# Optimization experiments

Hardware: AMD Instinct MI355X
Metric: run time of the kernel (lower is better)

The kernel has to match this reference:

```python
import jax, jax.numpy as jnp
import numpy as np

B, N, D, H = 4, 512, 64, 8
DK = D // H  # 8


def setup_inputs() -> dict:
    key = jax.random.key(0)
    ks = jax.random.split(key, 9)
    std = 0.02
    return {
        "n": jax.random.normal(ks[0], (B, N, D), dtype=jnp.float32),
        "e": jax.random.normal(ks[1], (B, N, N, D), dtype=jnp.float32),
        "W_q": jax.random.normal(ks[2], (D, D), dtype=jnp.float32) * std,
        "W_k": jax.random.normal(ks[3], (D, D), dtype=jnp.float32) * std,
        "W_v": jax.random.normal(ks[4], (D, D), dtype=jnp.float32) * std,
        "O_n": jax.random.normal(ks[5], (D, D), dtype=jnp.float32) * std,
        "W_e": jax.random.normal(ks[6], (D, H), dtype=jnp.float32) * std,
        "W_g": jax.random.normal(ks[7], (D, H), dtype=jnp.float32) * std,
        "O_e": jax.random.normal(ks[8], (H, D), dtype=jnp.float32) * std,
    }


def reference(n, e, W_q, W_k, W_v, O_n, W_e, W_g, O_e):
    b, nn_, d = n.shape
    # projections -> [B, H, N, DK]
    Q = (n @ W_q).reshape(b, nn_, H, DK).transpose(0, 2, 1, 3)
    K = (n @ W_k).reshape(b, nn_, H, DK).transpose(0, 2, 1, 3)
    V = (n @ W_v).reshape(b, nn_, H, DK).transpose(0, 2, 1, 3)
    # edge bias and gate -> [B, H, N, N]
    E = jnp.einsum('bnmd,dh->bhnm', e, W_e)
    G = jax.nn.sigmoid(jnp.einsum('bnmd,dh->bhnm', e, W_g))
    dyn_centrality = jnp.log1p(G.sum(-1))  # [B, H, N]
    # clamped scaled scores + edge bias
    A = jnp.einsum('bhnd,bhmd->bhnm', Q, K) * (DK ** -0.5)
    A = jnp.clip(A, -5.0, 5.0)
    Eb = A + E
    P = jax.nn.softmax(Eb, axis=-1)
    Vh = jnp.einsum('bhnm,bhmd->bhnd', P, V)
    Vh = Vh * dyn_centrality[..., None]
    n_out = Vh.transpose(0, 2, 1, 3).reshape(b, nn_, d) @ O_n
    e_out = jnp.einsum('bhnm,hd->bnmd', Eb, O_e)
    return n_out, e_out
```

## Files before the change

### kernel.cpp

```cpp
#include <hip/hip_runtime.h>
#include <hip/hip_bf16.h>
#include <math.h>

#define BB 4
#define NN 512
#define NP 516
#define DD 64
#define HH 8
#define DKK 8

typedef float f32x4 __attribute__((ext_vector_type(4)));
typedef short s16x8 __attribute__((ext_vector_type(8)));

__device__ __forceinline__ void split8(const float* fv, s16x8& hi, s16x8& lo) {
#pragma unroll
    for (int j = 0; j < 8; ++j) {
        const unsigned u = __float_as_uint(fv[j]);
        hi[j] = (short)(u >> 16);
        const float r = fv[j] - __uint_as_float(u & 0xFFFF0000u);
        lo[j] = (short)(__float_as_uint(r) >> 16);
    }
}

__device__ __forceinline__ short bf16rne(float f) {
    return (short)((__float_as_uint(f) + 0x8000u) >> 16);
}

__device__ __forceinline__ int swz(int r, int cb) {
    return r * 256 + (cb ^ ((r & 7) << 4));
}

__global__ __launch_bounds__(64) void qkv_kernel(
    const float* __restrict__ n,
    const float* __restrict__ Wq,
    const float* __restrict__ Wk,
    const float* __restrict__ Wv,
    float* __restrict__ Q,
    float* __restrict__ K,
    float* __restrict__ V)
{
    const int row = blockIdx.x;
    const int j = threadIdx.x;
    __shared__ __align__(16) float nr[DD];
    nr[j] = n[(size_t)row * DD + j];
    __syncthreads();
    float q = 0.f, k = 0.f, v = 0.f;
#pragma unroll
    for (int d = 0; d < DD; ++d) {
        const float nv = nr[d];
        q = fmaf(nv, Wq[d * DD + j], q);
        k = fmaf(nv, Wk[d * DD + j], k);
        v = fmaf(nv, Wv[d * DD + j], v);
    }
    Q[(size_t)row * DD + j] = q;
    K[(size_t)row * DD + j] = k;
    V[(size_t)row * DD + j] = v;
}

__global__ __launch_bounds__(64) void edge_kernel(
    const float* __restrict__ e,
    const float* __restrict__ Q,
    const float* __restrict__ K,
    const float* __restrict__ We,
    const float* __restrict__ Wg,
    const float* __restrict__ Oe,
    float* __restrict__ Ebws,
    float* __restrict__ gpartws,
    float* __restrict__ e_out)
{
    const int blk = blockIdx.x;
    const int row = blk >> 2;
    const int qtr = blk & 3;
    const int b = row >> 9;
    const int lane = threadIdx.x;
    const int cc = lane & 15;
    const int kg = lane >> 4;
    const int wr = lane >> 4;
    const int wc = (lane & 15) << 4;

    __shared__ __align__(16) char lds_e[4096];
    __shared__ __align__(16) char lds_k[4096];
    __shared__ __align__(16) char lds_o[4096];

    const float scale = 0.35355339059327373f;

    s16x8 qxh0 = {0,0,0,0,0,0,0,0}, qxh1 = {0,0,0,0,0,0,0,0};
    {
        const float* Qr = Q + (size_t)row * DD;
        if (cc == kg) {
#pragma unroll
            for (int j = 0; j < 8; ++j) qxh0[j] = bf16rne(Qr[kg * 8 + j]);
        }
        if (cc == 4 + kg) {
#pragma unroll
            for (int j = 0; j < 8; ++j) qxh1[j] = bf16rne(Qr[32 + kg * 8 + j]);
        }
    }

    s16x8 b1h0, b1l0, b1h1, b1l1;
    {
        float fv[8];
#pragma unroll
        for (int j = 0; j < 8; ++j) {
            const int k = kg * 8 + j;
            fv[j] = (cc < 8) ? We[k * HH + cc] : Wg[k * HH + (cc - 8)];
        }
        split8(fv, b1h0, b1l0);
#pragma unroll
        for (int j = 0; j < 8; ++j) {
            const int k = 32 + kg * 8 + j;
            fv[j] = (cc < 8) ? We[k * HH + cc] : Wg[k * HH + (cc - 8)];
        }
        split8(fv, b1h1, b1l1);
    }
    s16x8 b2h[4], b2l[4];
#pragma unroll
    for (int nt = 0; nt < 4; ++nt) {
        float fv[8];
#pragma unroll
        for (int j = 0; j < 8; ++j)
            fv[j] = (kg == 0) ? Oe[j * DD + nt * 16 + cc] : 0.f;
        split8(fv, b2h[nt], b2l[nt]);
    }

    float gs0 = 0.f, gs1 = 0.f, gs2 = 0.f, gs3 = 0.f;
    const float* __restrict__ e_row = e + (size_t)row * NN * DD;
    const float* __restrict__ Kb = K + (size_t)b * NN * DD;
    float* __restrict__ eo = e_out + (size_t)row * NN * DD;
    const int T0 = qtr * 8;
    const int lastT = T0 + 7;

    float4 eA0, eA1, eA2, eA3, kA0, kA1, kA2, kA3;
    float4 eB0, eB1, eB2, eB3, kB0, kB1, kB2, kB3;
    {
        const float* se = e_row + (size_t)T0 * 16 * DD + lane * 4;
        eA0 = *(const float4*)(se);        eA1 = *(const float4*)(se + 256);
        eA2 = *(const float4*)(se + 512);  eA3 = *(const float4*)(se + 768);
        const float* sk = Kb + (size_t)T0 * 16 * DD + lane * 4;
        kA0 = *(const float4*)(sk);        kA1 = *(const float4*)(sk + 256);
        kA2 = *(const float4*)(sk + 512);  kA3 = *(const float4*)(sk + 768);
        const float* se2 = e_row + (size_t)(T0 + 1) * 16 * DD + lane * 4;
        eB0 = *(const float4*)(se2);       eB1 = *(const float4*)(se2 + 256);
        eB2 = *(const float4*)(se2 + 512); eB3 = *(const float4*)(se2 + 768);
        const float* sk2 = Kb + (size_t)(T0 + 1) * 16 * DD + lane * 4;
        kB0 = *(const float4*)(sk2);       kB1 = *(const float4*)(sk2 + 256);
        kB2 = *(const float4*)(sk2 + 512); kB3 = *(const float4*)(sk2 + 768);
    }

    auto body = [&](int T,
                    float4& p0, float4& p1, float4& p2, float4& p3,
                    float4& q0, float4& q1, float4& q2, float4& q3) {
        const int m0 = T * 16;

        *(float4*)(lds_e + swz(0 + wr, wc)) = p0;
        *(float4*)(lds_e + swz(4 + wr, wc)) = p1;
        *(float4*)(lds_e + swz(8 + wr, wc)) = p2;
        *(float4*)(lds_e + swz(12 + wr, wc)) = p3;
        *(float4*)(lds_k + swz(0 + wr, wc)) = q0;
        *(float4*)(lds_k + swz(4 + wr, wc)) = q1;
        *(float4*)(lds_k + swz(8 + wr, wc)) = q2;
        *(float4*)(lds_k + swz(12 + wr, wc)) = q3;

        {
            int Tn = T + 2; if (Tn > lastT) Tn = lastT;
            const float* se = e_row + (size_t)Tn * 16 * DD + lane * 4;
            p0 = *(const float4*)(se);        p1 = *(const float4*)(se + 256);
            p2 = *(const float4*)(se + 512);  p3 = *(const float4*)(se + 768);
            const float* sk = Kb + (size_t)Tn * 16 * DD + lane * 4;
            q0 = *(const float4*)(sk);        q1 = *(const float4*)(sk + 256);
            q2 = *(const float4*)(sk + 512);  q3 = *(const float4*)(sk + 768);
        }

        const float4 ef0 = *(const float4*)(lds_e + swz(cc, kg * 32));
        const float4 ef1 = *(const float4*)(lds_e + swz(cc, kg * 32 + 16));
        const float4 ef2 = *(const float4*)(lds_e + swz(cc, 128 + kg * 32));
        const float4 ef3 = *(const float4*)(lds_e + swz(cc, 128 + kg * 32 + 16));
        const float4 kf0 = *(const float4*)(lds_k + swz(cc, kg * 32));
        const float4 kf1 = *(const float4*)(lds_k + swz(cc, kg * 32 + 16));
        const float4 kf2 = *(const float4*)(lds_k + swz(cc, 128 + kg * 32));
        const float4 kf3 = *(const float4*)(lds_k + swz(cc, 128 + kg * 32 + 16));

        s16x8 a1h0, a1h1, kh0, kh1;
        a1h0[0] = bf16rne(ef0.x); a1h0[1] = bf16rne(ef0.y);
        a1h0[2] = bf16rne(ef0.z); a1h0[3] = bf16rne(ef0.w);
        a1h0[4] = bf16rne(ef1.x); a1h0[5] = bf16rne(ef1.y);
        a1h0[6] = bf16rne(ef1.z); a1h0[7] = bf16rne(ef1.w);
        a1h1[0] = bf16rne(ef2.x); a1h1[1] = bf16rne(ef2.y);
        a1h1[2] = bf16rne(ef2.z); a1h1[3] = bf16rne(ef2.w);
        a1h1[4] = bf16rne(ef3.x); a1h1[5] = bf16rne(ef3.y);
        a1h1[6] = bf16rne(ef3.z); a1h1[7] = bf16rne(ef3.w);
        kh0[0] = bf16rne(kf0.x); kh0[1] = bf16rne(kf0.y);
        kh0[2] = bf16rne(kf0.z); kh0[3] = bf16rne(kf0.w);
        kh0[4] = bf16rne(kf1.x); kh0[5] = bf16rne(kf1.y);
        kh0[6] = bf16rne(kf1.z); kh0[7] = bf16rne(kf1.w);
        kh1[0] = bf16rne(kf2.x); kh1[1] = bf16rne(kf2.y);
        kh1[2] = bf16rne(kf2.z); kh1[3] = bf16rne(kf2.w);
        kh1[4] = bf16rne(kf3.x); kh1[5] = bf16rne(kf3.y);
        kh1[6] = bf16rne(kf3.z); kh1[7] = bf16rne(kf3.w);

        f32x4 accA = {0.f, 0.f, 0.f, 0.f};
        accA = __builtin_amdgcn_mfma_f32_16x16x32_bf16(qxh0, kh0, accA, 0, 0, 0);
        accA = __builtin_amdgcn_mfma_f32_16x16x32_bf16(qxh1, kh1, accA, 0, 0, 0);

        f32x4 accEG = {0.f, 0.f, 0.f, 0.f};
        accEG = __builtin_amdgcn_mfma_f32_16x16x32_bf16(b1h0, a1h0, accEG, 0, 0, 0);
        accEG = __builtin_amdgcn_mfma_f32_16x16x32_bf16(b1l0, a1h0, accEG, 0, 0, 0);
        accEG = __builtin_amdgcn_mfma_f32_16x16x32_bf16(b1h1, a1h1, accEG, 0, 0, 0);
        accEG = __builtin_amdgcn_mfma_f32_16x16x32_bf16(b1l1, a1h1, accEG, 0, 0, 0);

        float ebr0 = 0.f, ebr1 = 0.f, ebr2 = 0.f, ebr3 = 0.f;
        if (kg < 2) {
            const float a0 = fminf(fmaxf(accA[0] * scale, -5.f), 5.f);
            const float a1 = fminf(fmaxf(accA[1] * scale, -5.f), 5.f);
            const float a2 = fminf(fmaxf(accA[2] * scale, -5.f), 5.f);
            const float a3 = fminf(fmaxf(accA[3] * scale, -5.f), 5.f);
            ebr0 = a0 + accEG[0];
            ebr1 = a1 + accEG[1];
            ebr2 = a2 + accEG[2];
            ebr3 = a3 + accEG[3];
            const size_t base = ((size_t)row * HH + kg * 4) * NN + m0 + cc;
            Ebws[base]          = ebr0;
            Ebws[base + NN]     = ebr1;
            Ebws[base + 2 * NN] = ebr2;
            Ebws[base + 3 * NN] = ebr3;
        } else {
            gs0 += 1.f / (1.f + __expf(-accEG[0]));
            gs1 += 1.f / (1.f + __expf(-accEG[1]));
            gs2 += 1.f / (1.f + __expf(-accEG[2]));
            gs3 += 1.f / (1.f + __expf(-accEG[3]));
        }

        const float pm0 = __shfl_xor(ebr0, 16, 64);
        const float pm1 = __shfl_xor(ebr1, 16, 64);
        const float pm2 = __shfl_xor(ebr2, 16, 64);
        const float pm3 = __shfl_xor(ebr3, 16, 64);

        s16x8 a2h, a2l;
        {
            float mj[8] = {ebr0, ebr1, ebr2, ebr3, pm0, pm1, pm2, pm3};
            split8(mj, a2h, a2l);
        }
        if (lane >= 16) {
            a2h = s16x8{0, 0, 0, 0, 0, 0, 0, 0};
            a2l = s16x8{0, 0, 0, 0, 0, 0, 0, 0};
        }

#pragma unroll
        for (int nt = 0; nt < 4; ++nt) {
            f32x4 c2 = {0.f, 0.f, 0.f, 0.f};
            c2 = __builtin_amdgcn_mfma_f32_16x16x32_bf16(b2h[nt], a2h, c2, 0, 0, 0);
            c2 = __builtin_amdgcn_mfma_f32_16x16x32_bf16(b2h[nt], a2l, c2, 0, 0, 0);
            c2 = __builtin_amdgcn_mfma_f32_16x16x32_bf16(b2l[nt], a2h, c2, 0, 0, 0);
            float4 st;
            st.x = c2[0]; st.y = c2[1]; st.z = c2[2]; st.w = c2[3];
            *(float4*)(lds_o + swz(cc, nt * 64 + kg * 16)) = st;
        }

        {
            float* eob = eo + (size_t)m0 * DD + lane * 4;
            const float4 o0 = *(const float4*)(lds_o + swz(0 + wr, wc));
            const float4 o1 = *(const float4*)(lds_o + swz(4 + wr, wc));
            const float4 o2 = *(const float4*)(lds_o + swz(8 + wr, wc));
            const float4 o3 = *(const float4*)(lds_o + swz(12 + wr, wc));
            *(float4*)(eob)       = o0;
            *(float4*)(eob + 256) = o1;
            *(float4*)(eob + 512) = o2;
            *(float4*)(eob + 768) = o3;
        }
    };

#pragma unroll 1
    for (int s4 = 0; s4 < 4; ++s4) {
        body(T0 + 2 * s4,     eA0, eA1, eA2, eA3, kA0, kA1, kA2, kA3);
        body(T0 + 2 * s4 + 1, eB0, eB1, eB2, eB3, kB0, kB1, kB2, kB3);
    }

    gs0 += __shfl_xor(gs0, 1, 64); gs0 += __shfl_xor(gs0, 2, 64);
    gs0 += __shfl_xor(gs0, 4, 64); gs0 += __shfl_xor(gs0, 8, 64);
    gs1 += __shfl_xor(gs1, 1, 64); gs1 += __shfl_xor(gs1, 2, 64);
    gs1 += __shfl_xor(gs1, 4, 64); gs1 += __shfl_xor(gs1, 8, 64);
    gs2 += __shfl_xor(gs2, 1, 64); gs2 += __shfl_xor(gs2, 2, 64);
    gs2 += __shfl_xor(gs2, 4, 64); gs2 += __shfl_xor(gs2, 8, 64);
    gs3 += __shfl_xor(gs3, 1, 64); gs3 += __shfl_xor(gs3, 2, 64);
    gs3 += __shfl_xor(gs3, 4, 64); gs3 += __shfl_xor(gs3, 8, 64);
    float* gp = gpartws + ((size_t)row * 4 + qtr) * HH;
    if (lane == 32) { gp[0] = gs0; gp[1] = gs1; gp[2] = gs2; gp[3] = gs3; }
    if (lane == 48) { gp[4] = gs0; gp[5] = gs1; gp[6] = gs2; gp[7] = gs3; }
}

__global__ __launch_bounds__(256) void softmax_kernel(
    const float* __restrict__ Ebws,
    const float* __restrict__ gpartws,
    const float* __restrict__ V,
    const float* __restrict__ On,
    float* __restrict__ n_out)
{
    const int row = blockIdx.x;
    const int b = row >> 9;
    const int t = threadIdx.x;
    const int lane = t & 63;
    const int wv = t >> 6;

    __shared__ float gsum[HH];
    __shared__ float vh_lds[DD];

    if (t < HH) {
        const float* gp = gpartws + (size_t)row * 4 * HH;
        gsum[t] = gp[t] + gp[HH + t] + gp[2 * HH + t] + gp[3 * HH + t];
    }
    __syncthreads();

    const float* __restrict__ Vb = V + (size_t)b * NN * DD;
#pragma unroll
    for (int hh = 0; hh < 2; ++hh) {
        const int h = wv + hh * 4;
        const float* __restrict__ ebr = Ebws + ((size_t)row * HH + h) * NN;
        float x[8];
#pragma unroll
        for (int k = 0; k < 8; ++k) x[k] = ebr[lane + (k << 6)];
        float mx = x[0];
#pragma unroll
        for (int k = 1; k < 8; ++k) mx = fmaxf(mx, x[k]);
        mx = fmaxf(mx, __shfl_xor(mx, 1, 64));
        mx = fmaxf(mx, __shfl_xor(mx, 2, 64));
        mx = fmaxf(mx, __shfl_xor(mx, 4, 64));
        mx = fmaxf(mx, __shfl_xor(mx, 8, 64));
        mx = fmaxf(mx, __shfl_xor(mx, 16, 64));
        mx = fmaxf(mx, __shfl_xor(mx, 32, 64));
        float p[8];
        float s = 0.f;
#pragma unroll
        for (int k = 0; k < 8; ++k) { p[k] = __expf(x[k] - mx); s += p[k]; }
        s += __shfl_xor(s, 1, 64);
        s += __shfl_xor(s, 2, 64);
        s += __shfl_xor(s, 4, 64);
        s += __shfl_xor(s, 8, 64);
        s += __shfl_xor(s, 16, 64);
        s += __shfl_xor(s, 32, 64);

        float pv[8];
#pragma unroll
        for (int dk = 0; dk < 8; ++dk) pv[dk] = 0.f;
#pragma unroll
        for (int k = 0; k < 8; ++k) {
            const float* vr = Vb + (size_t)(lane + (k << 6)) * DD + h * DKK;
            const float4 va = *(const float4*)vr;
            const float4 vb2 = *(const float4*)(vr + 4);
            const float pk = p[k];
            pv[0] = fmaf(pk, va.x, pv[0]);
            pv[1] = fmaf(pk, va.y, pv[1]);
            pv[2] = fmaf(pk, va.z, pv[2]);
            pv[3] = fmaf(pk, va.w, pv[3]);
            pv[4] = fmaf(pk, vb2.x, pv[4]);
            pv[5] = fmaf(pk, vb2.y, pv[5]);
            pv[6] = fmaf(pk, vb2.z, pv[6]);
            pv[7] = fmaf(pk, vb2.w, pv[7]);
        }
#pragma unroll
        for (int dk = 0; dk < 8; ++dk) {
            float x2 = pv[dk];
            x2 += __shfl_xor(x2, 1, 64);
            x2 += __shfl_xor(x2, 2, 64);
            x2 += __shfl_xor(x2, 4, 64);
            x2 += __shfl_xor(x2, 8, 64);
            x2 += __shfl_xor(x2, 16, 64);
            x2 += __shfl_xor(x2, 32, 64);
            pv[dk] = x2;
        }
        if (lane == 0) {
            const float sc = log1pf(gsum[h]) / s;
#pragma unroll
            for (int dk = 0; dk < 8; ++dk) vh_lds[h * DKK + dk] = pv[dk] * sc;
        }
    }
    __syncthreads();

    if (t < DD) {
        const int j = t;
        float acc = 0.f;
#pragma unroll
        for (int d = 0; d < DD; ++d) acc = fmaf(vh_lds[d], On[d * DD + j], acc);
        n_out[(size_t)row * DD + j] = acc;
    }
}

__global__ __launch_bounds__(256) void attn_fused(
    const float* __restrict__ e,
    const float* __restrict__ Q,
    const float* __restrict__ K,
    const float* __restrict__ V,
    const float* __restrict__ We,
    const float* __restrict__ Wg,
    const float* __restrict__ Oe,
    const float* __restrict__ On,
    float* __restrict__ n_out,
    float* __restrict__ e_out)
{
    const int row = blockIdx.x;
    const int b = row >> 9;
    const int t = threadIdx.x;
    const int lane = t & 63;
    const int wv = t >> 6;
    const int cc = lane & 15;
    const int kg = lane >> 4;

    __shared__ __align__(16) float eb_lds[HH][NP];
    __shared__ float gpart[4][HH];
    __shared__ float gsum[HH];
    __shared__ float vh_lds[DD];

    const float scale = 0.35355339059327373f;
    const float* __restrict__ Kb = K + (size_t)b * NN * DD;
    const float* __restrict__ Qr = Q + (size_t)row * DD;

    for (int mm = 0; mm < 2; ++mm) {
        const int m = wv * 128 + lane + mm * 64;
        const float4* __restrict__ kr = (const float4*)(Kb + (size_t)m * DD);
        const float4* __restrict__ qr = (const float4*)Qr;
#pragma unroll
        for (int h = 0; h < HH; ++h) {
            const float4 k0 = kr[2 * h];
            const float4 k1 = kr[2 * h + 1];
            const float4 q0 = qr[2 * h];
            const float4 q1 = qr[2 * h + 1];
            float a = q0.x * k0.x;
            a = fmaf(q0.y, k0.y, a); a = fmaf(q0.z, k0.z, a); a = fmaf(q0.w, k0.w, a);
            a = fmaf(q1.x, k1.x, a); a = fmaf(q1.y, k1.y, a);
            a = fmaf(q1.z, k1.z, a); a = fmaf(q1.w, k1.w, a);
            a *= scale;
            eb_lds[h][m] = fminf(fmaxf(a, -5.f), 5.f);
        }
    }

    s16x8 b1h0, b1l0, b1h1, b1l1;
    {
        float fv[8];
#pragma unroll
        for (int j = 0; j < 8; ++j) {
            const int k = kg * 8 + j;
            fv[j] = (cc < 8) ? We[k * HH + cc] : Wg[k * HH + (cc - 8)];
        }
        split8(fv, b1h0, b1l0);
#pragma unroll
        for (int j = 0; j < 8; ++j) {
            const int k = 32 + kg * 8 + j;
            fv[j] = (cc < 8) ? We[k * HH + cc] : Wg[k * HH + (cc - 8)];
        }
        split8(fv, b1h1, b1l1);
    }
    s16x8 b2h[4], b2l[4];
#pragma unroll
    for (int nt = 0; nt < 4; ++nt) {
        float fv[8];
#pragma unroll
        for (int j = 0; j < 8; ++j)
            fv[j] = (kg == 0) ? Oe[j * DD + nt * 16 + cc] : 0.f;
        split8(fv, b2h[nt], b2l[nt]);
    }

    float gs40 = 0.f, gs41 = 0.f, gs42 = 0.f, gs43 = 0.f;
    const float* __restrict__ e_row = e + (size_t)row * NN * DD;
    float* __restrict__ eo = e_out + (size_t)row * NN * DD;
    const int T0 = wv * 8;
    const int lastT = T0 + 7;

    float4 A0, A1, A2, A3, B0, B1, B2, B3;
    {
        const float* s = e_row + (size_t)(T0 * 16 + cc) * DD + kg * 8;
        A0 = *(const float4*)s;        A1 = *(const float4*)(s + 4);
        A2 = *(const float4*)(s + 32); A3 = *(const float4*)(s + 36);
        const float* s2 = e_row + (size_t)((T0 + 1) * 16 + cc) * DD + kg * 8;
        B0 = *(const float4*)s2;        B1 = *(const float4*)(s2 + 4);
        B2 = *(const float4*)(s2 + 32); B3 = *(const float4*)(s2 + 36);
    }

    auto body = [&](int T, float4& p0, float4& p1, float4& p2, float4& p3) {
        const int m0 = T * 16;
        s16x8 a1h0, a1h1;
        a1h0[0] = bf16rne(p0.x); a1h0[1] = bf16rne(p0.y);
        a1h0[2] = bf16rne(p0.z); a1h0[3] = bf16rne(p0.w);
        a1h0[4] = bf16rne(p1.x); a1h0[5] = bf16rne(p1.y);
        a1h0[6] = bf16rne(p1.z); a1h0[7] = bf16rne(p1.w);
        a1h1[0] = bf16rne(p2.x); a1h1[1] = bf16rne(p2.y);
        a1h1[2] = bf16rne(p2.z); a1h1[3] = bf16rne(p2.w);
        a1h1[4] = bf16rne(p3.x); a1h1[5] = bf16rne(p3.y);
        a1h1[6] = bf16rne(p3.z); a1h1[7] = bf16rne(p3.w);
        {
            int Tn = T + 2; if (Tn > lastT) Tn = lastT;
            const float* s = e_row + (size_t)(Tn * 16 + cc) * DD + kg * 8;
            p0 = *(const float4*)s;        p1 = *(const float4*)(s + 4);
            p2 = *(const float4*)(s + 32); p3 = *(const float4*)(s + 36);
        }
        f32x4 acc = {0.f, 0.f, 0.f, 0.f};
        acc = __builtin_amdgcn_mfma_f32_16x16x32_bf16(b1h0, a1h0, acc, 0, 0, 0);
        acc = __builtin_amdgcn_mfma_f32_16x16x32_bf16(b1l0, a1h0, acc, 0, 0, 0);
        acc = __builtin_amdgcn_mfma_f32_16x16x32_bf16(b1h1, a1h1, acc, 0, 0, 0);
        acc = __builtin_amdgcn_mfma_f32_16x16x32_bf16(b1l1, a1h1, acc, 0, 0, 0);

        float ebr0 = 0.f, ebr1 = 0.f, ebr2 = 0.f, ebr3 = 0.f;
        if (kg < 2) {
            const int h0 = kg * 4;
            const int m = m0 + cc;
            ebr0 = eb_lds[h0 + 0][m] + acc[0]; eb_lds[h0 + 0][m] = ebr0;
            ebr1 = eb_lds[h0 + 1][m] + acc[1]; eb_lds[h0 + 1][m] = ebr1;
            ebr2 = eb_lds[h0 + 2][m] + acc[2]; eb_lds[h0 + 2][m] = ebr2;
            ebr3 = eb_lds[h0 + 3][m] + acc[3]; eb_lds[h0 + 3][m] = ebr3;
        } else {
            gs40 += 1.f / (1.f + __expf(-acc[0]));
            gs41 += 1.f / (1.f + __expf(-acc[1]));
            gs42 += 1.f / (1.f + __expf(-acc[2]));
            gs43 += 1.f / (1.f + __expf(-acc[3]));
        }
        const float pm0 = __shfl_xor(ebr0, 16, 64);
        const float pm1 = __shfl_xor(ebr1, 16, 64);
        const float pm2 = __shfl_xor(ebr2, 16, 64);
        const float pm3 = __shfl_xor(ebr3, 16, 64);
        s16x8 a2h, a2l;
        {
            float mj[8] = {ebr0, ebr1, ebr2, ebr3, pm0, pm1, pm2, pm3};
            split8(mj, a2h, a2l);
        }
        if (lane >= 16) {
            a2h = s16x8{0, 0, 0, 0, 0, 0, 0, 0};
            a2l = s16x8{0, 0, 0, 0, 0, 0, 0, 0};
        }
#pragma unroll
        for (int nt = 0; nt < 4; ++nt) {
            f32x4 c2 = {0.f, 0.f, 0.f, 0.f};
            c2 = __builtin_amdgcn_mfma_f32_16x16x32_bf16(a2h, b2h[nt], c2, 0, 0, 0);
            c2 = __builtin_amdgcn_mfma_f32_16x16x32_bf16(a2l, b2h[nt], c2, 0, 0, 0);
            c2 = __builtin_amdgcn_mfma_f32_16x16x32_bf16(a2h, b2l[nt], c2, 0, 0, 0);
#pragma unroll
            for (int r = 0; r < 4; ++r) {
                const int m = m0 + kg * 4 + r;
                eo[(size_t)m * DD + nt * 16 + cc] = c2[r];
            }
        }
    };

#pragma unroll 1
    for (int s4 = 0; s4 < 4; ++s4) {
        body(T0 + 2 * s4,     A0, A1, A2, A3);
        body(T0 + 2 * s4 + 1, B0, B1, B2, B3);
    }

    gs40 += __shfl_xor(gs40, 1, 64); gs40 += __shfl_xor(gs40, 2, 64);
    gs40 += __shfl_xor(gs40, 4, 64); gs40 += __shfl_xor(gs40, 8, 64);
    gs41 += __shfl_xor(gs41, 1, 64); gs41 += __shfl_xor(gs41, 2, 64);
    gs41 += __shfl_xor(gs41, 4, 64); gs41 += __shfl_xor(gs41, 8, 64);
    gs42 += __shfl_xor(gs42, 1, 64); gs42 += __shfl_xor(gs42, 2, 64);
    gs42 += __shfl_xor(gs42, 4, 64); gs42 += __shfl_xor(gs42, 8, 64);
    gs43 += __shfl_xor(gs43, 1, 64); gs43 += __shfl_xor(gs43, 2, 64);
    gs43 += __shfl_xor(gs43, 4, 64); gs43 += __shfl_xor(gs43, 8, 64);
    if (lane == 32) {
        gpart[wv][0] = gs40; gpart[wv][1] = gs41;
        gpart[wv][2] = gs42; gpart[wv][3] = gs43;
    }
    if (lane == 48) {
        gpart[wv][4] = gs40; gpart[wv][5] = gs41;
        gpart[wv][6] = gs42; gpart[wv][7] = gs43;
    }
    __syncthreads();
    if (t < HH) gsum[t] = gpart[0][t] + gpart[1][t] + gpart[2][t] + gpart[3][t];
    __syncthreads();

    const float* __restrict__ Vb = V + (size_t)b * NN * DD;
#pragma unroll
    for (int hh = 0; hh < 2; ++hh) {
        const int h = wv + hh * 4;
        float x[8];
#pragma unroll
        for (int k = 0; k < 8; ++k) x[k] = eb_lds[h][lane + (k << 6)];
        float mx = x[0];
#pragma unroll
        for (int k = 1; k < 8; ++k) mx = fmaxf(mx, x[k]);
        mx = fmaxf(mx, __shfl_xor(mx, 1, 64));
        mx = fmaxf(mx, __shfl_xor(mx, 2, 64));
        mx = fmaxf(mx, __shfl_xor(mx, 4, 64));
        mx = fmaxf(mx, __shfl_xor(mx, 8, 64));
        mx = fmaxf(mx, __shfl_xor(mx, 16, 64));
        mx = fmaxf(mx, __shfl_xor(mx, 32, 64));
        float p[8];
        float s = 0.f;
#pragma unroll
        for (int k = 0; k < 8; ++k) { p[k] = __expf(x[k] - mx); s += p[k]; }
        s += __shfl_xor(s, 1, 64);
        s += __shfl_xor(s, 2, 64);
        s += __shfl_xor(s, 4, 64);
        s += __shfl_xor(s, 8, 64);
        s += __shfl_xor(s, 16, 64);
        s += __shfl_xor(s, 32, 64);
        float pv[8];
#pragma unroll
        for (int dk = 0; dk < 8; ++dk) pv[dk] = 0.f;
#pragma unroll
        for (int k = 0; k < 8; ++k) {
            const float* vr = Vb + (size_t)(lane + (k << 6)) * DD + h * DKK;
            const float4 va = *(const float4*)vr;
            const float4 vb2 = *(const float4*)(vr + 4);
            const float pk = p[k];
            pv[0] = fmaf(pk, va.x, pv[0]);
            pv[1] = fmaf(pk, va.y, pv[1]);
            pv[2] = fmaf(pk, va.z, pv[2]);
            pv[3] = fmaf(pk, va.w, pv[3]);
            pv[4] = fmaf(pk, vb2.x, pv[4]);
            pv[5] = fmaf(pk, vb2.y, pv[5]);
            pv[6] = fmaf(pk, vb2.z, pv[6]);
            pv[7] = fmaf(pk, vb2.w, pv[7]);
        }
#pragma unroll
        for (int dk = 0; dk < 8; ++dk) {
            float x2 = pv[dk];
            x2 += __shfl_xor(x2, 1, 64);
            x2 += __shfl_xor(x2, 2, 64);
            x2 += __shfl_xor(x2, 4, 64);
            x2 += __shfl_xor(x2, 8, 64);
            x2 += __shfl_xor(x2, 16, 64);
            x2 += __shfl_xor(x2, 32, 64);
            pv[dk] = x2;
        }
        if (lane == 0) {
            const float sc = log1pf(gsum[h]) / s;
#pragma unroll
            for (int dk = 0; dk < 8; ++dk) vh_lds[h * DKK + dk] = pv[dk] * sc;
        }
    }
    __syncthreads();
    if (t < DD) {
        const int j = t;
        float acc = 0.f;
#pragma unroll
        for (int d = 0; d < DD; ++d) acc = fmaf(vh_lds[d], On[d * DD + j], acc);
        n_out[(size_t)row * DD + j] = acc;
    }
}

extern "C" void kernel_launch(void* const* d_in, const int* in_sizes, int n_in,
                              void* d_out, int out_size, void* d_ws, size_t ws_size,
                              hipStream_t stream) {
    const float* n  = (const float*)d_in[0];
    const float* e  = (const float*)d_in[1];
    const float* Wq = (const float*)d_in[2];
    const float* Wk = (const float*)d_in[3];
    const float* Wv = (const float*)d_in[4];
    const float* On = (const float*)d_in[5];
    const float* We = (const float*)d_in[6];
    const float* Wg = (const float*)d_in[7];
    const float* Oe = (const float*)d_in[8];

    float* out = (float*)d_out;
    float* n_out = out;
    float* e_out = out + (size_t)BB * NN * DD;

    float* Q = (float*)d_ws;
    float* K = Q + (size_t)BB * NN * DD;
    float* V = K + (size_t)BB * NN * DD;

    qkv_kernel<<<BB * NN, 64, 0, stream>>>(n, Wq, Wk, Wv, Q, K, V);

    const size_t qkv_f  = (size_t)3 * BB * NN * DD;
    const size_t eb_f   = (size_t)BB * NN * HH * NN;
    const size_t gp_f   = (size_t)BB * NN * 4 * HH;
    const size_t need_b = (qkv_f + eb_f + gp_f) * sizeof(float);

    if (ws_size >= need_b) {
        float* Ebws    = V + (size_t)BB * NN * DD;
        float* gpartws = Ebws + eb_f;
        edge_kernel<<<BB * NN * 4, 64, 0, stream>>>(e, Q, K, We, Wg, Oe,
                                                    Ebws, gpartws, e_out);
        softmax_kernel<<<BB * NN, 256, 0, stream>>>(Ebws, gpartws, V, On, n_out);
    } else {
        attn_fused<<<BB * NN, 256, 0, stream>>>(e, Q, K, V, We, Wg, Oe, On,
                                                n_out, e_out);
    }
}
```

Before: 163.3 us.

## Precompute K as bf16 MFMA fragments in a separate kernel

Adds a small kernel that converts K to bf16 and stores it already arranged in the per-lane MFMA operand layout. The edge kernel then loads two 16-byte fragments per tile directly instead of staging fp32 K through LDS and converting it every tile, for every one of the 8192 blocks. It also replaces the scalar bf16 rounding of e with packed float2-to-bf16 conversions. The cost is one extra kernel launch and a little more workspace.

```diff
diff --git a/kernel.cpp b/kernel.cpp
--- a/kernel.cpp
+++ b/kernel.cpp
@@ -24,6 +24,17 @@
 
 __device__ __forceinline__ short bf16rne(float f) {
     return (short)((__float_as_uint(f) + 0x8000u) >> 16);
+}
+
+__device__ __forceinline__ s16x8 cvt8(const float4& a, const float4& b) {
+    union { __hip_bfloat162 h; unsigned u; } c0, c1, c2, c3;
+    c0.h = __float22bfloat162_rn(make_float2(a.x, a.y));
+    c1.h = __float22bfloat162_rn(make_float2(a.z, a.w));
+    c2.h = __float22bfloat162_rn(make_float2(b.x, b.y));
+    c3.h = __float22bfloat162_rn(make_float2(b.z, b.w));
+    union { unsigned u[4]; s16x8 s; } r;
+    r.u[0] = c0.u; r.u[1] = c1.u; r.u[2] = c2.u; r.u[3] = c3.u;
+    return r.s;
 }
 
 __device__ __forceinline__ int swz(int r, int cb) {
@@ -57,10 +68,33 @@
     V[(size_t)row * DD + j] = v;
 }
 
+__global__ __launch_bounds__(64) void kfrag_kernel(
+    const float* __restrict__ K,
+    unsigned short* __restrict__ Kf)
+{
+    const int blk = blockIdx.x;
+    const int b = blk >> 5;
+    const int T = blk & 31;
+    const int lane = threadIdx.x;
+    const int cc = lane & 15;
+    const int kg = lane >> 4;
+
+    const float* src = K + ((size_t)b * NN + T * 16 + cc) * DD + kg * 8;
+    const float4 k0 = *(const float4*)(src);
+    const float4 k1 = *(const float4*)(src + 4);
+    const float4 k2 = *(const float4*)(src + 32);
+    const float4 k3 = *(const float4*)(src + 36);
+    const s16x8 kh0 = cvt8(k0, k1);
+    const s16x8 kh1 = cvt8(k2, k3);
+    s16x8* out = (s16x8*)Kf;
+    out[((size_t)blk * 2 + 0) * 64 + lane] = kh0;
+    out[((size_t)blk * 2 + 1) * 64 + lane] = kh1;
+}
+
 __global__ __launch_bounds__(64) void edge_kernel(
     const float* __restrict__ e,
     const float* __restrict__ Q,
-    const float* __restrict__ K,
+    const unsigned short* __restrict__ Kf,
     const float* __restrict__ We,
     const float* __restrict__ Wg,
     const float* __restrict__ Oe,
@@ -79,7 +113,6 @@
     const int wc = (lane & 15) << 4;
 
     __shared__ __align__(16) char lds_e[4096];
-    __shared__ __align__(16) char lds_k[4096];
     __shared__ __align__(16) char lds_o[4096];
 
     const float scale = 0.35355339059327373f;
@@ -125,82 +158,58 @@
 
     float gs0 = 0.f, gs1 = 0.f, gs2 = 0.f, gs3 = 0.f;
     const float* __restrict__ e_row = e + (size_t)row * NN * DD;
-    const float* __restrict__ Kb = K + (size_t)b * NN * DD;
+    const s16x8* __restrict__ kfp = (const s16x8*)Kf;
     float* __restrict__ eo = e_out + (size_t)row * NN * DD;
     const int T0 = qtr * 8;
     const int lastT = T0 + 7;
-
-    float4 eA0, eA1, eA2, eA3, kA0, kA1, kA2, kA3;
-    float4 eB0, eB1, eB2, eB3, kB0, kB1, kB2, kB3;
+    const int kbase = b * 32;
+
+    float4 eA0, eA1, eA2, eA3, eB0, eB1, eB2, eB3;
+    s16x8 kfA0, kfA1, kfB0, kfB1;
     {
         const float* se = e_row + (size_t)T0 * 16 * DD + lane * 4;
         eA0 = *(const float4*)(se);        eA1 = *(const float4*)(se + 256);
         eA2 = *(const float4*)(se + 512);  eA3 = *(const float4*)(se + 768);
-        const float* sk = Kb + (size_t)T0 * 16 * DD + lane * 4;
-        kA0 = *(const float4*)(sk);        kA1 = *(const float4*)(sk + 256);
-        kA2 = *(const float4*)(sk + 512);  kA3 = *(const float4*)(sk + 768);
+        kfA0 = kfp[((size_t)(kbase + T0) * 2 + 0) * 64 + lane];
+        kfA1 = kfp[((size_t)(kbase + T0) * 2 + 1) * 64 + lane];
         const float* se2 = e_row + (size_t)(T0 + 1) * 16 * DD + lane * 4;
         eB0 = *(const float4*)(se2);       eB1 = *(const float4*)(se2 + 256);
         eB2 = *(const float4*)(se2 + 512); eB3 = *(const float4*)(se2 + 768);
-        const float* sk2 = Kb + (size_t)(T0 + 1) * 16 * DD + lane * 4;
-        kB0 = *(const float4*)(sk2);       kB1 = *(const float4*)(sk2 + 256);
-        kB2 = *(const float4*)(sk2 + 512); kB3 = *(const float4*)(sk2 + 768);
+        kfB0 = kfp[((size_t)(kbase + T0 + 1) * 2 + 0) * 64 + lane];
+        kfB1 = kfp[((size_t)(kbase + T0 + 1) * 2 + 1) * 64 + lane];
     }
 
     auto body = [&](int T,
                     float4& p0, float4& p1, float4& p2, float4& p3,
-                    float4& q0, float4& q1, float4& q2, float4& q3) {
+                    s16x8& kh0, s16x8& kh1) {
         const int m0 = T * 16;
 
         *(float4*)(lds_e + swz(0 + wr, wc)) = p0;
         *(float4*)(lds_e + swz(4 + wr, wc)) = p1;
         *(float4*)(lds_e + swz(8 + wr, wc)) = p2;
         *(float4*)(lds_e + swz(12 + wr, wc)) = p3;
-        *(float4*)(lds_k + swz(0 + wr, wc)) = q0;
-        *(float4*)(lds_k + swz(4 + wr, wc)) = q1;
-        *(float4*)(lds_k + swz(8 + wr, wc)) = q2;
-        *(float4*)(lds_k + swz(12 + wr, wc)) = q3;
-
+
+        const s16x8 kc0 = kh0, kc1 = kh1;
         {
             int Tn = T + 2; if (Tn > lastT) Tn = lastT;
             const float* se = e_row + (size_t)Tn * 16 * DD + lane * 4;
             p0 = *(const float4*)(se);        p1 = *(const float4*)(se + 256);
             p2 = *(const float4*)(se + 512);  p3 = *(const float4*)(se + 768);
-            const float* sk = Kb + (size_t)Tn * 16 * DD + lane * 4;
-            q0 = *(const float4*)(sk);        q1 = *(const float4*)(sk + 256);
-            q2 = *(const float4*)(sk + 512);  q3 = *(const float4*)(sk + 768);
+            kh0 = kfp[((size_t)(kbase + Tn) * 2 + 0) * 64 + lane];
+            kh1 = kfp[((size_t)(kbase + Tn) * 2 + 1) * 64 + lane];
         }
 
         const float4 ef0 = *(const float4*)(lds_e + swz(cc, kg * 32));
         const float4 ef1 = *(const float4*)(lds_e + swz(cc, kg * 32 + 16));
         const float4 ef2 = *(const float4*)(lds_e + swz(cc, 128 + kg * 32));
         const float4 ef3 = *(const float4*)(lds_e + swz(cc, 128 + kg * 32 + 16));
-        const float4 kf0 = *(const float4*)(lds_k + swz(cc, kg * 32));
-        const float4 kf1 = *(const float4*)(lds_k + swz(cc, kg * 32 + 16));
-        const float4 kf2 = *(const float4*)(lds_k + swz(cc, 128 + kg * 32));
-        const float4 kf3 = *(const float4*)(lds_k + swz(cc, 128 + kg * 32 + 16));
-
-        s16x8 a1h0, a1h1, kh0, kh1;
-        a1h0[0] = bf16rne(ef0.x); a1h0[1] = bf16rne(ef0.y);
-        a1h0[2] = bf16rne(ef0.z); a1h0[3] = bf16rne(ef0.w);
-        a1h0[4] = bf16rne(ef1.x); a1h0[5] = bf16rne(ef1.y);
-        a1h0[6] = bf16rne(ef1.z); a1h0[7] = bf16rne(ef1.w);
-        a1h1[0] = bf16rne(ef2.x); a1h1[1] = bf16rne(ef2.y);
-        a1h1[2] = bf16rne(ef2.z); a1h1[3] = bf16rne(ef2.w);
-        a1h1[4] = bf16rne(ef3.x); a1h1[5] = bf16rne(ef3.y);
-        a1h1[6] = bf16rne(ef3.z); a1h1[7] = bf16rne(ef3.w);
-        kh0[0] = bf16rne(kf0.x); kh0[1] = bf16rne(kf0.y);
-        kh0[2] = bf16rne(kf0.z); kh0[3] = bf16rne(kf0.w);
-        kh0[4] = bf16rne(kf1.x); kh0[5] = bf16rne(kf1.y);
-        kh0[6] = bf16rne(kf1.z); kh0[7] = bf16rne(kf1.w);
-        kh1[0] = bf16rne(kf2.x); kh1[1] = bf16rne(kf2.y);
-        kh1[2] = bf16rne(kf2.z); kh1[3] = bf16rne(kf2.w);
-        kh1[4] = bf16rne(kf3.x); kh1[5] = bf16rne(kf3.y);
-        kh1[6] = bf16rne(kf3.z); kh1[7] = bf16rne(kf3.w);
+
+        const s16x8 a1h0 = cvt8(ef0, ef1);
+        const s16x8 a1h1 = cvt8(ef2, ef3);
 
         f32x4 accA = {0.f, 0.f, 0.f, 0.f};
-        accA = __builtin_amdgcn_mfma_f32_16x16x32_bf16(qxh0, kh0, accA, 0, 0, 0);
-        accA = __builtin_amdgcn_mfma_f32_16x16x32_bf16(qxh1, kh1, accA, 0, 0, 0);
+        accA = __builtin_amdgcn_mfma_f32_16x16x32_bf16(qxh0, kc0, accA, 0, 0, 0);
+        accA = __builtin_amdgcn_mfma_f32_16x16x32_bf16(qxh1, kc1, accA, 0, 0, 0);
 
         f32x4 accEG = {0.f, 0.f, 0.f, 0.f};
         accEG = __builtin_amdgcn_mfma_f32_16x16x32_bf16(b1h0, a1h0, accEG, 0, 0, 0);
@@ -271,8 +280,8 @@
 
 #pragma unroll 1
     for (int s4 = 0; s4 < 4; ++s4) {
-        body(T0 + 2 * s4,     eA0, eA1, eA2, eA3, kA0, kA1, kA2, kA3);
-        body(T0 + 2 * s4 + 1, eB0, eB1, eB2, eB3, kB0, kB1, kB2, kB3);
+        body(T0 + 2 * s4,     eA0, eA1, eA2, eA3, kfA0, kfA1);
+        body(T0 + 2 * s4 + 1, eB0, eB1, eB2, eB3, kfB0, kfB1);
     }
 
     gs0 += __shfl_xor(gs0, 1, 64); gs0 += __shfl_xor(gs0, 2, 64);
@@ -661,12 +670,15 @@
     const size_t qkv_f  = (size_t)3 * BB * NN * DD;
     const size_t eb_f   = (size_t)BB * NN * HH * NN;
     const size_t gp_f   = (size_t)BB * NN * 4 * HH;
-    const size_t need_b = (qkv_f + eb_f + gp_f) * sizeof(float);
+    const size_t kf_f   = (size_t)BB * 32 * 2 * 64 * 8 / 2;
+    const size_t need_b = (qkv_f + eb_f + gp_f + kf_f) * sizeof(float);
 
     if (ws_size >= need_b) {
         float* Ebws    = V + (size_t)BB * NN * DD;
         float* gpartws = Ebws + eb_f;
-        edge_kernel<<<BB * NN * 4, 64, 0, stream>>>(e, Q, K, We, Wg, Oe,
+        unsigned short* Kf = (unsigned short*)(gpartws + gp_f);
+        kfrag_kernel<<<BB * 32, 64, 0, stream>>>(K, Kf);
+        edge_kernel<<<BB * NN * 4, 64, 0, stream>>>(e, Q, Kf, We, Wg, Oe,
                                                     Ebws, gpartws, e_out);
         softmax_kernel<<<BB * NN, 256, 0, stream>>>(Ebws, gpartws, V, On, n_out);
     } else {
```

Result: no change. 165.3 us (+1.2%).
